# Performance work log

Hardware: AMD Instinct MI355X
Metric: run time of the kernel (lower is better)

The kernel has to match this reference:

```python
import jax, jax.numpy as jnp
import numpy as np

INPUT_DIM = 1024
OUTPUT_DIM = 1024
DEGREE = 8
N_TOKENS = 8192


def setup_inputs() -> dict:
    key = jax.random.key(0)
    k1, k2 = jax.random.split(key)
    x = jax.random.normal(k1, (N_TOKENS, INPUT_DIM), dtype=jnp.float32)
    # xavier_normal_ with gain = 1/(input_dim*(degree+1)) over fan dims (output_dim, degree+1)
    fan_in, fan_out = OUTPUT_DIM, DEGREE + 1  # torch treats dim0/dim1 as fans; scale is tiny anyway
    gain = 1.0 / (INPUT_DIM * (DEGREE + 1))
    std = gain * np.sqrt(2.0 / (INPUT_DIM + OUTPUT_DIM))
    cheby_coeffs = std * jax.random.normal(k2, (INPUT_DIM, OUTPUT_DIM, DEGREE + 1), dtype=jnp.float32)
    return {"x": x, "cheby_coeffs": cheby_coeffs}


def reference(x, cheby_coeffs):
    # x: (..., input_dim) -> y: (..., output_dim)
    degree_p1 = cheby_coeffs.shape[-1]
    theta = jnp.arccos(jnp.tanh(x))                      # (..., i)
    arange = jnp.arange(degree_p1, dtype=x.dtype)        # (d,)
    basis = jnp.cos(theta[..., None] * arange)           # (..., i, d) Chebyshev T_d(tanh(x))
    y = jnp.einsum('...id,iod->...o', basis, cheby_coeffs)
    return y
```

## Files before the change

kernel.cpp:

```cpp
#include <hip/hip_runtime.h>


typedef __bf16 bf16;
typedef __bf16 bf16x8 __attribute__((ext_vector_type(8)));
typedef float f32x2 __attribute__((ext_vector_type(2)));
typedef float f32x4 __attribute__((ext_vector_type(4)));
typedef float f32x16 __attribute__((ext_vector_type(16)));

#define MFMA __builtin_amdgcn_mfma_f32_32x32x16_bf16

__device__ __forceinline__ void g2lds16(const void* g, void* l) {
  __builtin_amdgcn_global_load_lds(
      (const __attribute__((address_space(1))) unsigned int*)g,
      (__attribute__((address_space(3))) unsigned int*)l, 16, 0, 0);
}

__device__ __forceinline__ float fast_tanh(float a) {
  float e = __expf(a + a);
  return 1.f - 2.f * __builtin_amdgcn_rcpf(e + 1.f);
}

__global__ __launch_bounds__(256)
void cheby_prep3(const float* __restrict__ x, const float* __restrict__ C,
                 bf16* __restrict__ A, bf16* __restrict__ B,
                 float* __restrict__ bias_p) {
  const int bid = blockIdx.x, tid = threadIdx.x;
  if (bid < 2048) {
    const int rb = bid >> 4, ig = bid & 15;
    const int rl = tid & 63, ih = tid >> 6;
    const int i_base = ig * 64 + ih * 16;
    const int mb = rb >> 1;
    const int rs = (rb & 1) * 64 + rl;
    const int m32 = rs >> 5, ml = rs & 31;
    const float* xp = x + (size_t)(rb * 64 + rl) * 1024 + i_base;
    bf16* aout = A + (size_t)mb * 1048576;
    #pragma unroll
    for (int q = 0; q < 4; ++q) {
      f32x4 xv = *(const f32x4*)(xp + q * 4);
      #pragma unroll
      for (int j = 0; j < 4; ++j) {
        const int ia = i_base + q * 4 + j;
        const int kt = ia >> 3, cc = ia & 7;
        float z = fast_tanh(xv[j]);
        float z2 = z + z, pv = 1.f, cv = z;
        bf16x8 v;
        #pragma unroll
        for (int d = 0; d < 8; ++d) {
          v[d] = (bf16)cv;
          float nx = z2 * cv - pv; pv = cv; cv = nx;
        }
        const int widx = (((cc >> 1) * 4 + m32) * 2 + (cc & 1)) * 32 + ml;
        *(bf16x8*)(aout + (size_t)kt * 8192 + widx * 8) = v;
      }
    }
    return;
  }
  const int b2 = bid - 2048;
  __shared__ float tile[32][292];
  const int i0 = (b2 >> 5) * 32, o0 = (b2 & 31) * 32;
  {
    const int r = tid >> 3, seg = tid & 7;
    const float* src = C + (size_t)(i0 + r) * 9216 + (size_t)o0 * 9 + seg * 36;
    float* dst = &tile[r][seg * 36];
    #pragma unroll
    for (int v = 0; v < 9; ++v) *(f32x4*)(dst + v * 4) = *(const f32x4*)(src + v * 4);
  }
  __syncthreads();
  #pragma unroll
  for (int j = 0; j < 4; ++j) {
    int e = tid + 256 * j;
    int il = e >> 5, ol = e & 31;
    int i = i0 + il, o = o0 + ol;
    bf16x8 v;
    #pragma unroll
    for (int d = 0; d < 8; ++d) v[d] = (bf16)tile[il][ol * 9 + 1 + d];
    const int cc = i & 7;
    size_t tnum = (size_t)(o >> 7) * 128 + (i >> 3);
    const int widx = (((cc >> 1) * 4 + ((o & 127) >> 5)) * 2 + (cc & 1)) * 32 + (o & 31);
    *(bf16x8*)(B + tnum * 8192 + widx * 8) = v;
  }
  if (tid < 32) {
    float s = 0.f;
    #pragma unroll
    for (int i = 0; i < 32; ++i) s += tile[i][tid * 9];
    bias_p[(size_t)(b2 >> 5) * 1024 + o0 + tid] = s;
  }
}

__global__ __launch_bounds__(512, 1)
void cheby_gemm4(const bf16* __restrict__ A, const bf16* __restrict__ B,
                 const float* __restrict__ bias_p, float* __restrict__ out) {
  __shared__ bf16 ring[3][24576];
  const int tid = threadIdx.x;
  const int lane = tid & 63, w = tid >> 6;
  const int wm = w >> 1, wn = w & 1;
  const int bid = blockIdx.x;
  const int wgid = (bid & 7) * 32 + (bid >> 3);
  const int mb2 = wgid >> 3, nb = wgid & 7;

  const int ml = lane & 31, h = lane >> 5;
  const int aLane = h * 256 + ml * 8;
  const int row0 = wm * 64, row1 = row0 + 32;
  const int aBase0 = (row0 >> 7) * 8192 + ((row0 >> 5) & 3) * 512 + aLane;
  const int aBase1 = (row1 >> 7) * 8192 + ((row1 >> 5) & 3) * 512 + aLane;
  const int bBase  = 16384 + wn * 1024 + aLane;

  const bf16* aG = A + (size_t)(mb2 * 2) * 1048576 + tid * 8;
  const bf16* bG = B + (size_t)nb * 1048576 + tid * 8;

  f32x16 acc[2][2];
  #pragma unroll
  for (int a = 0; a < 2; ++a)
    #pragma unroll
    for (int b = 0; b < 2; ++b)
      #pragma unroll
      for (int r = 0; r < 16; ++r) acc[a][b][r] = 0.f;

  auto issueA01 = [&](int t, int p) {
    g2lds16(aG + (size_t)t * 8192,        &ring[p][tid * 8]);
    g2lds16(aG + (size_t)t * 8192 + 4096, &ring[p][4096 + tid * 8]);
  };
  auto issueA23B = [&](int t, int p) {
    g2lds16(aG + 1048576 + (size_t)t * 8192,        &ring[p][8192 + tid * 8]);
    g2lds16(aG + 1048576 + (size_t)t * 8192 + 4096, &ring[p][12288 + tid * 8]);
    g2lds16(bG + (size_t)t * 8192,                  &ring[p][16384 + tid * 8]);
    g2lds16(bG + (size_t)t * 8192 + 4096,           &ring[p][20480 + tid * 8]);
  };

  issueA01(0, 0); issueA23B(0, 0);
  issueA01(1, 1); issueA23B(1, 1);
  asm volatile("s_waitcnt vmcnt(6)" ::: "memory");
  __builtin_amdgcn_s_barrier();

  auto step = [&](int t, int pc, int pn) {
    const bf16* ra = &ring[pc][0];
    const bool pf = (t + 2 < 128);
    {
      bf16x8 a00 = *(const bf16x8*)(ra + aBase0);
      bf16x8 a10 = *(const bf16x8*)(ra + aBase1);
      bf16x8 a01 = *(const bf16x8*)(ra + aBase0 + 2048);
      bf16x8 a11 = *(const bf16x8*)(ra + aBase1 + 2048);
      bf16x8 b00 = *(const bf16x8*)(ra + bBase);
      bf16x8 b10 = *(const bf16x8*)(ra + bBase + 512);
      bf16x8 b01 = *(const bf16x8*)(ra + bBase + 2048);
      bf16x8 b11 = *(const bf16x8*)(ra + bBase + 2048 + 512);
      if (pf) issueA01(t + 2, pn);
      __builtin_amdgcn_s_barrier();
      __builtin_amdgcn_s_setprio(1);
      acc[0][0] = MFMA(a00, b00, acc[0][0], 0, 0, 0);
      acc[0][1] = MFMA(a00, b10, acc[0][1], 0, 0, 0);
      acc[1][0] = MFMA(a10, b00, acc[1][0], 0, 0, 0);
      acc[1][1] = MFMA(a10, b10, acc[1][1], 0, 0, 0);
      acc[0][0] = MFMA(a01, b01, acc[0][0], 0, 0, 0);
      acc[0][1] = MFMA(a01, b11, acc[0][1], 0, 0, 0);
      acc[1][0] = MFMA(a11, b01, acc[1][0], 0, 0, 0);
      acc[1][1] = MFMA(a11, b11, acc[1][1], 0, 0, 0);
      __builtin_amdgcn_s_setprio(0);
      __builtin_amdgcn_s_barrier();
    }
    {
      bf16x8 a02 = *(const bf16x8*)(ra + aBase0 + 4096);
      bf16x8 a12 = *(const bf16x8*)(ra + aBase1 + 4096);
      bf16x8 a03 = *(const bf16x8*)(ra + aBase0 + 4096 + 2048);
      bf16x8 a13 = *(const bf16x8*)(ra + aBase1 + 4096 + 2048);
      bf16x8 b02 = *(const bf16x8*)(ra + bBase + 4096);
      bf16x8 b12 = *(const bf16x8*)(ra + bBase + 4096 + 512);
      bf16x8 b03 = *(const bf16x8*)(ra + bBase + 4096 + 2048);
      bf16x8 b13 = *(const bf16x8*)(ra + bBase + 4096 + 2048 + 512);
      if (pf) issueA23B(t + 2, pn);
      if (t < 126) asm volatile("s_waitcnt vmcnt(6)" ::: "memory");
      else         asm volatile("s_waitcnt vmcnt(0)" ::: "memory");
      __builtin_amdgcn_s_barrier();
      __builtin_amdgcn_s_setprio(1);
      acc[0][0] = MFMA(a02, b02, acc[0][0], 0, 0, 0);
      acc[0][1] = MFMA(a02, b12, acc[0][1], 0, 0, 0);
      acc[1][0] = MFMA(a12, b02, acc[1][0], 0, 0, 0);
      acc[1][1] = MFMA(a12, b12, acc[1][1], 0, 0, 0);
      acc[0][0] = MFMA(a03, b03, acc[0][0], 0, 0, 0);
      acc[0][1] = MFMA(a03, b13, acc[0][1], 0, 0, 0);
      acc[1][0] = MFMA(a13, b03, acc[1][0], 0, 0, 0);
      acc[1][1] = MFMA(a13, b13, acc[1][1], 0, 0, 0);
      __builtin_amdgcn_s_setprio(0);
      __builtin_amdgcn_s_barrier();
    }
  };

  #pragma unroll 1
  for (int t3 = 0; t3 < 126; t3 += 3) {
    step(t3,     0, 2);
    step(t3 + 1, 1, 0);
    step(t3 + 2, 2, 1);
  }
  step(126, 0, 2);
  step(127, 1, 0);

  const int c0 = nb * 128 + wn * 64 + ml;
  float bv0 = 0.f, bv1 = 0.f;
  #pragma unroll
  for (int p = 0; p < 32; ++p) {
    bv0 += bias_p[(size_t)p * 1024 + c0];
    bv1 += bias_p[(size_t)p * 1024 + c0 + 32];
  }
  const int r0 = mb2 * 256 + wm * 64;
  #pragma unroll
  for (int mt = 0; mt < 2; ++mt)
    #pragma unroll
    for (int r = 0; r < 16; ++r) {
      int row = r0 + mt * 32 + (r & 3) + 8 * (r >> 2) + 4 * h;
      float* po = out + (size_t)row * 1024 + c0;
      po[0]  = acc[mt][0][r] + bv0;
      po[32] = acc[mt][1][r] + bv1;
    }
}

__global__ __launch_bounds__(256)
void cheby_naive(const float* __restrict__ x, const float* __restrict__ C,
                 float* __restrict__ out) {
  const int t = blockIdx.x, tid = threadIdx.x;
  float acc[4] = {0.f, 0.f, 0.f, 0.f};
  for (int i = 0; i < 1024; ++i) {
    float th = tanhf(x[(size_t)t * 1024 + i]);
    float T[9]; T[0] = 1.f; T[1] = th;
    #pragma unroll
    for (int d = 2; d < 9; ++d) T[d] = 2.f * th * T[d - 1] - T[d - 2];
    #pragma unroll
    for (int j = 0; j < 4; ++j) {
      const float* cp = &C[((size_t)i * 1024 + tid + j * 256) * 9];
      float s = 0.f;
      #pragma unroll
      for (int d = 0; d < 9; ++d) s += T[d] * cp[d];
      acc[j] += s;
    }
  }
  #pragma unroll
  for (int j = 0; j < 4; ++j) out[(size_t)t * 1024 + tid + j * 256] = acc[j];
}

extern "C" void kernel_launch(void* const* d_in, const int* in_sizes, int n_in,
                              void* d_out, int out_size, void* d_ws, size_t ws_size,
                              hipStream_t stream) {
  (void)in_sizes; (void)n_in; (void)out_size;
  const float* x = (const float*)d_in[0];
  const float* C = (const float*)d_in[1];
  float* out = (float*)d_out;

  const size_t a_bytes  = (size_t)8192 * 8192 * 2;
  const size_t b_bytes  = (size_t)8 * 128 * 8192 * 2;
  const size_t bp_bytes = (size_t)32 * 1024 * 4;

  if (ws_size >= a_bytes + b_bytes + bp_bytes) {
    bf16*  A      = (bf16*)d_ws;
    bf16*  B      = (bf16*)((char*)d_ws + a_bytes);
    float* bias_p = (float*)((char*)d_ws + a_bytes + b_bytes);
    cheby_prep3<<<3072, 256, 0, stream>>>(x, C, A, B, bias_p);
    cheby_gemm4<<<256, 512, 0, stream>>>(A, B, bias_p, out);
  } else {
    cheby_naive<<<8192, 256, 0, stream>>>(x, C, out);
  }
}
```

Before: 254.4 us.

## Register-double-buffer GEMM fragments with prefetch depth 3; stage x through LDS in prep

```diff
diff --git a/kernel.cpp b/kernel.cpp
--- a/kernel.cpp
+++ b/kernel.cpp
@@ -21,27 +21,35 @@
 }
 
 __global__ __launch_bounds__(256)
-void cheby_prep3(const float* __restrict__ x, const float* __restrict__ C,
+void cheby_prep4(const float* __restrict__ x, const float* __restrict__ C,
                  bf16* __restrict__ A, bf16* __restrict__ B,
                  float* __restrict__ bias_p) {
   const int bid = blockIdx.x, tid = threadIdx.x;
   if (bid < 2048) {
+    __shared__ float xs[64][65];
     const int rb = bid >> 4, ig = bid & 15;
+    #pragma unroll
+    for (int it = 0; it < 4; ++it) {
+      const int e = tid + it * 256;
+      const int rr = e >> 4, c4 = (e & 15) * 4;
+      f32x4 v = *(const f32x4*)(x + (size_t)(rb * 64 + rr) * 1024 + ig * 64 + c4);
+      xs[rr][c4 + 0] = v.x; xs[rr][c4 + 1] = v.y;
+      xs[rr][c4 + 2] = v.z; xs[rr][c4 + 3] = v.w;
+    }
+    __syncthreads();
     const int rl = tid & 63, ih = tid >> 6;
-    const int i_base = ig * 64 + ih * 16;
     const int mb = rb >> 1;
     const int rs = (rb & 1) * 64 + rl;
     const int m32 = rs >> 5, ml = rs & 31;
-    const float* xp = x + (size_t)(rb * 64 + rl) * 1024 + i_base;
     bf16* aout = A + (size_t)mb * 1048576;
     #pragma unroll
     for (int q = 0; q < 4; ++q) {
-      f32x4 xv = *(const f32x4*)(xp + q * 4);
       #pragma unroll
       for (int j = 0; j < 4; ++j) {
-        const int ia = i_base + q * 4 + j;
+        const int il = ih * 16 + q * 4 + j;
+        const int ia = ig * 64 + il;
         const int kt = ia >> 3, cc = ia & 7;
-        float z = fast_tanh(xv[j]);
+        float z = fast_tanh(xs[rl][il]);
         float z2 = z + z, pv = 1.f, cv = z;
         bf16x8 v;
         #pragma unroll
@@ -88,7 +96,7 @@
 }
 
 __global__ __launch_bounds__(512, 1)
-void cheby_gemm4(const bf16* __restrict__ A, const bf16* __restrict__ B,
+void cheby_gemm5(const bf16* __restrict__ A, const bf16* __restrict__ B,
                  const float* __restrict__ bias_p, float* __restrict__ out) {
   __shared__ bf16 ring[3][24576];
   const int tid = threadIdx.x;
@@ -116,83 +124,67 @@
       #pragma unroll
       for (int r = 0; r < 16; ++r) acc[a][b][r] = 0.f;
 
-  auto issueA01 = [&](int t, int p) {
-    g2lds16(aG + (size_t)t * 8192,        &ring[p][tid * 8]);
-    g2lds16(aG + (size_t)t * 8192 + 4096, &ring[p][4096 + tid * 8]);
-  };
-  auto issueA23B = [&](int t, int p) {
+  struct F { bf16x8 a0[4], a1[4], b0[4], b1[4]; };
+  F f0, f1;
+
+  auto issueB6 = [&](int t, int p) {
+    g2lds16(aG + (size_t)t * 8192,                  &ring[p][tid * 8]);
+    g2lds16(aG + (size_t)t * 8192 + 4096,           &ring[p][4096 + tid * 8]);
     g2lds16(aG + 1048576 + (size_t)t * 8192,        &ring[p][8192 + tid * 8]);
     g2lds16(aG + 1048576 + (size_t)t * 8192 + 4096, &ring[p][12288 + tid * 8]);
     g2lds16(bG + (size_t)t * 8192,                  &ring[p][16384 + tid * 8]);
     g2lds16(bG + (size_t)t * 8192 + 4096,           &ring[p][20480 + tid * 8]);
   };
-
-  issueA01(0, 0); issueA23B(0, 0);
-  issueA01(1, 1); issueA23B(1, 1);
+  auto loadFrags = [&](F& f, const bf16* ra) {
+    #pragma unroll
+    for (int ks = 0; ks < 4; ++ks) {
+      const int off = (ks & 1) * 2048 + (ks >> 1) * 4096;
+      f.a0[ks] = *(const bf16x8*)(ra + aBase0 + off);
+      f.a1[ks] = *(const bf16x8*)(ra + aBase1 + off);
+      f.b0[ks] = *(const bf16x8*)(ra + bBase + off);
+      f.b1[ks] = *(const bf16x8*)(ra + bBase + off + 512);
+    }
+  };
+  auto mfma16 = [&](F& c) {
+    __builtin_amdgcn_s_setprio(1);
+    #pragma unroll
+    for (int ks = 0; ks < 4; ++ks) {
+      acc[0][0] = MFMA(c.a0[ks], c.b0[ks], acc[0][0], 0, 0, 0);
+      acc[0][1] = MFMA(c.a0[ks], c.b1[ks], acc[0][1], 0, 0, 0);
+      acc[1][0] = MFMA(c.a1[ks], c.b0[ks], acc[1][0], 0, 0, 0);
+      acc[1][1] = MFMA(c.a1[ks], c.b1[ks], acc[1][1], 0, 0, 0);
+    }
+    __builtin_amdgcn_s_setprio(0);
+  };
+
+  issueB6(0, 0); issueB6(1, 1); issueB6(2, 2);
   asm volatile("s_waitcnt vmcnt(6)" ::: "memory");
   __builtin_amdgcn_s_barrier();
-
-  auto step = [&](int t, int pc, int pn) {
-    const bf16* ra = &ring[pc][0];
-    const bool pf = (t + 2 < 128);
-    {
-      bf16x8 a00 = *(const bf16x8*)(ra + aBase0);
-      bf16x8 a10 = *(const bf16x8*)(ra + aBase1);
-      bf16x8 a01 = *(const bf16x8*)(ra + aBase0 + 2048);
-      bf16x8 a11 = *(const bf16x8*)(ra + aBase1 + 2048);
-      bf16x8 b00 = *(const bf16x8*)(ra + bBase);
-      bf16x8 b10 = *(const bf16x8*)(ra + bBase + 512);
-      bf16x8 b01 = *(const bf16x8*)(ra + bBase + 2048);
-      bf16x8 b11 = *(const bf16x8*)(ra + bBase + 2048 + 512);
-      if (pf) issueA01(t + 2, pn);
-      __builtin_amdgcn_s_barrier();
-      __builtin_amdgcn_s_setprio(1);
-      acc[0][0] = MFMA(a00, b00, acc[0][0], 0, 0, 0);
-      acc[0][1] = MFMA(a00, b10, acc[0][1], 0, 0, 0);
-      acc[1][0] = MFMA(a10, b00, acc[1][0], 0, 0, 0);
-      acc[1][1] = MFMA(a10, b10, acc[1][1], 0, 0, 0);
-      acc[0][0] = MFMA(a01, b01, acc[0][0], 0, 0, 0);
-      acc[0][1] = MFMA(a01, b11, acc[0][1], 0, 0, 0);
-      acc[1][0] = MFMA(a11, b01, acc[1][0], 0, 0, 0);
-      acc[1][1] = MFMA(a11, b11, acc[1][1], 0, 0, 0);
-      __builtin_amdgcn_s_setprio(0);
-      __builtin_amdgcn_s_barrier();
-    }
-    {
-      bf16x8 a02 = *(const bf16x8*)(ra + aBase0 + 4096);
-      bf16x8 a12 = *(const bf16x8*)(ra + aBase1 + 4096);
-      bf16x8 a03 = *(const bf16x8*)(ra + aBase0 + 4096 + 2048);
-      bf16x8 a13 = *(const bf16x8*)(ra + aBase1 + 4096 + 2048);
-      bf16x8 b02 = *(const bf16x8*)(ra + bBase + 4096);
-      bf16x8 b12 = *(const bf16x8*)(ra + bBase + 4096 + 512);
-      bf16x8 b03 = *(const bf16x8*)(ra + bBase + 4096 + 2048);
-      bf16x8 b13 = *(const bf16x8*)(ra + bBase + 4096 + 2048 + 512);
-      if (pf) issueA23B(t + 2, pn);
-      if (t < 126) asm volatile("s_waitcnt vmcnt(6)" ::: "memory");
-      else         asm volatile("s_waitcnt vmcnt(0)" ::: "memory");
-      __builtin_amdgcn_s_barrier();
-      __builtin_amdgcn_s_setprio(1);
-      acc[0][0] = MFMA(a02, b02, acc[0][0], 0, 0, 0);
-      acc[0][1] = MFMA(a02, b12, acc[0][1], 0, 0, 0);
-      acc[1][0] = MFMA(a12, b02, acc[1][0], 0, 0, 0);
-      acc[1][1] = MFMA(a12, b12, acc[1][1], 0, 0, 0);
-      acc[0][0] = MFMA(a03, b03, acc[0][0], 0, 0, 0);
-      acc[0][1] = MFMA(a03, b13, acc[0][1], 0, 0, 0);
-      acc[1][0] = MFMA(a13, b03, acc[1][0], 0, 0, 0);
-      acc[1][1] = MFMA(a13, b13, acc[1][1], 0, 0, 0);
-      __builtin_amdgcn_s_setprio(0);
-      __builtin_amdgcn_s_barrier();
-    }
+  loadFrags(f0, &ring[0][0]);
+  asm volatile("s_waitcnt lgkmcnt(0)" ::: "memory");
+  __builtin_amdgcn_s_barrier();
+
+  auto step = [&](int t, int bufI, int bufR, F& cur, F& nxt, bool rd) {
+    if (t + 3 < 128) issueB6(t + 3, bufI);
+    if (rd) loadFrags(nxt, &ring[bufR][0]);
+    mfma16(cur);
+    asm volatile("s_waitcnt lgkmcnt(0)" ::: "memory");
+    if (t < 125) asm volatile("s_waitcnt vmcnt(6)" ::: "memory");
+    else         asm volatile("s_waitcnt vmcnt(0)" ::: "memory");
+    __builtin_amdgcn_s_barrier();
   };
 
   #pragma unroll 1
-  for (int t3 = 0; t3 < 126; t3 += 3) {
-    step(t3,     0, 2);
-    step(t3 + 1, 1, 0);
-    step(t3 + 2, 2, 1);
-  }
-  step(126, 0, 2);
-  step(127, 1, 0);
+  for (int t6 = 0; t6 < 126; t6 += 6) {
+    step(t6 + 0, 0, 1, f0, f1, true);
+    step(t6 + 1, 1, 2, f1, f0, true);
+    step(t6 + 2, 2, 0, f0, f1, true);
+    step(t6 + 3, 0, 1, f1, f0, true);
+    step(t6 + 4, 1, 2, f0, f1, true);
+    step(t6 + 5, 2, 0, f1, f0, true);
+  }
+  step(126, 0, 1, f0, f1, true);
+  step(127, 1, 2, f1, f0, false);
 
   const int c0 = nb * 128 + wn * 64 + ml;
   float bv0 = 0.f, bv1 = 0.f;
@@ -252,8 +244,8 @@
     bf16*  A      = (bf16*)d_ws;
     bf16*  B      = (bf16*)((char*)d_ws + a_bytes);
     float* bias_p = (float*)((char*)d_ws + a_bytes + b_bytes);
-    cheby_prep3<<<3072, 256, 0, stream>>>(x, C, A, B, bias_p);
-    cheby_gemm4<<<256, 512, 0, stream>>>(A, B, bias_p, out);
+    cheby_prep4<<<3072, 256, 0, stream>>>(x, C, A, B, bias_p);
+    cheby_gemm5<<<256, 512, 0, stream>>>(A, B, bias_p, out);
   } else {
     cheby_naive<<<8192, 256, 0, stream>>>(x, C, out);
   }
```

After: 250.1 us. About the same (-1.7%).
